# Kernel optimization log

Measured on AMD Instinct MI355X. Metric: run time of the kernel, lower is better.

Reference implementation:

```python
import jax, jax.numpy as jnp
import numpy as np

N = 1024
IN_F = 256
OUT_F = 128
H = 4
NH = OUT_F // H  # 32
NEG_SLOPE = 0.2


def setup_inputs() -> dict:
    key = jax.random.key(0)
    k1, k2, k3, k4, k5 = jax.random.split(key, 5)
    h = jax.random.normal(k1, (N, IN_F), dtype=jnp.float32)
    adj_mat = jax.random.randint(k2, (N, N, 1), 0, 2, dtype=jnp.int32)
    s_in = 1.0 / np.sqrt(IN_F)
    s_nh = 1.0 / np.sqrt(NH)
    Wl = jax.random.uniform(k3, (H * NH, IN_F), jnp.float32, -s_in, s_in)
    Wr = jax.random.uniform(k4, (H * NH, IN_F), jnp.float32, -s_in, s_in)
    attn_w = jax.random.uniform(k5, (NH,), jnp.float32, -s_nh, s_nh)
    return {"h": h, "adj_mat": adj_mat, "Wl": Wl, "Wr": Wr, "attn_w": attn_w}


def reference(h, adj_mat, Wl, Wr, attn_w):
    n = h.shape[0]
    g_l = (h @ Wl.T).reshape(n, H, NH)  # [N,H,F]
    g_r = (h @ Wr.T).reshape(n, H, NH)  # [N,H,F]
    # g_sum[i, j] = g_l[j] + g_r[i]  (repeat / repeat_interleave semantics)
    g_sum = g_l[None, :, :, :] + g_r[:, None, :, :]  # [N,N,H,F]
    act = jnp.where(g_sum >= 0, g_sum, NEG_SLOPE * g_sum)
    e = jnp.einsum('ijhf,f->ijh', act, attn_w)  # [N,N,H]
    mask = adj_mat != 0  # [N,N,1] broadcasts over heads
    e = jnp.where(mask, e, -jnp.inf)
    a = jax.nn.softmax(e, axis=1)  # softmax over source nodes j
    h_prime = jnp.einsum('ijh,jhf->ihf', a, g_r).reshape(n, H * NH)
    # is_output_layer=False -> ELU (dropout is a no-op in eval)
    return jax.nn.elu(h_prime)
```

## Files before the change

kernel.cpp:

```cpp
#include <hip/hip_runtime.h>
#include <math.h>

#define NN 1024
#define IN_F 256
#define OUT_F 128
#define NHEADS 4
#define NHF 32
#define ITILE 4
#define HPSTR 260

__global__ void __launch_bounds__(256, 4) glr_gemm(const float* __restrict__ hmat,
                                                   const float* __restrict__ Wl,
                                                   const float* __restrict__ Wr,
                                                   float* __restrict__ glh,
                                                   float* __restrict__ grh) {
    __shared__ float hp[16 * HPSTR];
    const int tid = threadIdx.x;
    const int rg = blockIdx.x & 63;
    const int cs = blockIdx.x >> 6;

    const float4* __restrict__ hsrc = (const float4*)hmat + rg * (16 * 64);
#pragma unroll
    for (int i = 0; i < 4; ++i) {
        const int v = tid + i * 256;
        const int row = v >> 6, kq = v & 63;
        *(float4*)(hp + row * HPSTR + kq * 4) = hsrc[v];
    }
    __syncthreads();

    const int lane = tid & 63;
    const int row  = lane & 15;
    const int kc   = lane >> 4;
    const int wu   = __builtin_amdgcn_readfirstlane(tid >> 6);
    const int c0   = cs * 16 + wu * 4;
    const float* __restrict__ wb = (c0 < OUT_F) ? (Wl + c0 * IN_F)
                                                : (Wr + (c0 - OUT_F) * IN_F);
    const float* __restrict__ hrow = hp + row * HPSTR + kc * 64;
    const float* __restrict__ wrow = wb + kc * 64;

    float a0 = 0.f, a1 = 0.f, a2 = 0.f, a3 = 0.f;
#pragma unroll 4
    for (int i = 0; i < 16; ++i) {
        const float4 hv = *(const float4*)(hrow + i * 4);
        const float4 w0 = *(const float4*)(wrow + 0 * IN_F + i * 4);
        const float4 w1 = *(const float4*)(wrow + 1 * IN_F + i * 4);
        const float4 w2 = *(const float4*)(wrow + 2 * IN_F + i * 4);
        const float4 w3 = *(const float4*)(wrow + 3 * IN_F + i * 4);
        a0 = fmaf(hv.x, w0.x, fmaf(hv.y, w0.y, fmaf(hv.z, w0.z, fmaf(hv.w, w0.w, a0))));
        a1 = fmaf(hv.x, w1.x, fmaf(hv.y, w1.y, fmaf(hv.z, w1.z, fmaf(hv.w, w1.w, a1))));
        a2 = fmaf(hv.x, w2.x, fmaf(hv.y, w2.y, fmaf(hv.z, w2.z, fmaf(hv.w, w2.w, a2))));
        a3 = fmaf(hv.x, w3.x, fmaf(hv.y, w3.y, fmaf(hv.z, w3.z, fmaf(hv.w, w3.w, a3))));
    }
    a0 += __shfl_xor(a0, 16); a0 += __shfl_xor(a0, 32);
    a1 += __shfl_xor(a1, 16); a1 += __shfl_xor(a1, 32);
    a2 += __shfl_xor(a2, 16); a2 += __shfl_xor(a2, 32);
    a3 += __shfl_xor(a3, 16); a3 += __shfl_xor(a3, 32);

    if (kc == 0) {
        const int cb = c0 & (OUT_F - 1);
        const int hh = cb >> 5;
        const int f  = cb & 31;
        float* __restrict__ dst = (c0 < OUT_F) ? glh : grh;
        float4 r; r.x = a0; r.y = a1; r.z = a2; r.w = a3;
        *(float4*)(dst + (hh * NN + rg * 16 + row) * NHF + f) = r;
    }
}

__global__ void __launch_bounds__(512, 8) gat_main(const float* __restrict__ glh,
                                                   const float* __restrict__ grh,
                                                   const int* __restrict__ adj,
                                                   const float* __restrict__ attn_w,
                                                   float* __restrict__ out) {
    const int hh  = blockIdx.y;
    const int i0  = blockIdx.x * ITILE;
    const int tid = threadIdx.x;

    __shared__ float p_buf[ITILE][1028];
    __shared__ float part[ITILE][16][NHF];
    __shared__ float red[ITILE][8];
    __shared__ float l_sh[ITILE];

    float lpart[ITILE];
#pragma unroll
    for (int ii = 0; ii < ITILE; ++ii) lpart[ii] = 0.f;

#pragma unroll 1
    for (int c = 0; c < 2; ++c) {
        const int j = (c << 9) + tid;
        const float* __restrict__ gp = glh + (hh * NN + j) * NHF;
        int adjv[ITILE];
#pragma unroll
        for (int ii = 0; ii < ITILE; ++ii) adjv[ii] = adj[(i0 + ii) * NN + j];

        float S[ITILE];
#pragma unroll
        for (int ii = 0; ii < ITILE; ++ii) S[ii] = 0.f;
        float alpha = 0.f;

#pragma unroll
        for (int fh = 0; fh < 2; ++fh) {
            const int fb = fh << 4;
            float g[16];
#pragma unroll
            for (int f4 = 0; f4 < 4; ++f4) {
                const float4 v = *(const float4*)(gp + fb + (f4 << 2));
                g[4 * f4 + 0] = v.x; g[4 * f4 + 1] = v.y;
                g[4 * f4 + 2] = v.z; g[4 * f4 + 3] = v.w;
            }
#pragma unroll
            for (int k = 0; k < 16; ++k) alpha = fmaf(g[k], attn_w[fb + k], alpha);
#pragma unroll
            for (int ii = 0; ii < ITILE; ++ii) {
                const float* __restrict__ grp = grh + (hh * NN + i0 + ii) * NHF + fb;
                float s = S[ii];
#pragma unroll
                for (int k = 0; k < 16; ++k)
                    s = fmaf(fabsf(g[k] + grp[k]), attn_w[fb + k], s);
                S[ii] = s;
            }
        }
#pragma unroll
        for (int ii = 0; ii < ITILE; ++ii) {
            const float e = fmaf(0.4f, S[ii], 0.6f * alpha);
            const float p = adjv[ii] ? __expf(e) : 0.f;
            p_buf[ii][j] = p;
            lpart[ii] += p;
        }
    }

    const int lane = tid & 63, wv = tid >> 6;
#pragma unroll
    for (int ii = 0; ii < ITILE; ++ii) {
        float v = lpart[ii];
#pragma unroll
        for (int d = 32; d > 0; d >>= 1) v += __shfl_xor(v, d);
        if (lane == 0) red[ii][wv] = v;
    }
    __syncthreads();
    if (tid < ITILE) {
        float l = red[tid][0];
#pragma unroll
        for (int w = 1; w < 8; ++w) l += red[tid][w];
        l_sh[tid] = l;
    }
    __syncthreads();

    const int f  = tid & 31;
    const int js = tid >> 5;
    const float* __restrict__ gp = grh + hh * NN * NHF + f;
    float o[ITILE];
#pragma unroll
    for (int ii = 0; ii < ITILE; ++ii) o[ii] = 0.f;
    const int jb = js << 6;
#pragma unroll 4
    for (int jj = 0; jj < 64; jj += 4) {
        const int j = jb + jj;
        const float g0 = gp[(j + 0) * NHF];
        const float g1 = gp[(j + 1) * NHF];
        const float g2 = gp[(j + 2) * NHF];
        const float g3 = gp[(j + 3) * NHF];
#pragma unroll
        for (int ii = 0; ii < ITILE; ++ii) {
            const float4 p4 = *(const float4*)&p_buf[ii][j];
            o[ii] = fmaf(p4.x, g0, fmaf(p4.y, g1, fmaf(p4.z, g2, fmaf(p4.w, g3, o[ii]))));
        }
    }
#pragma unroll
    for (int ii = 0; ii < ITILE; ++ii) part[ii][js][f] = o[ii];
    __syncthreads();

    if (tid < 32 * ITILE) {
        const int ii = tid >> 5, ff = tid & 31;
        float s0 = 0.f, s1 = 0.f, s2 = 0.f, s3 = 0.f;
#pragma unroll
        for (int k = 0; k < 16; k += 4) {
            s0 += part[ii][k + 0][ff];
            s1 += part[ii][k + 1][ff];
            s2 += part[ii][k + 2][ff];
            s3 += part[ii][k + 3][ff];
        }
        float s = ((s0 + s1) + (s2 + s3)) / l_sh[ii];
        const float r = (s > 0.f) ? s : (__expf(s) - 1.f);
        out[(i0 + ii) * OUT_F + hh * NHF + ff] = r;
    }
}

extern "C" void kernel_launch(void* const* d_in, const int* in_sizes, int n_in,
                              void* d_out, int out_size, void* d_ws, size_t ws_size,
                              hipStream_t stream) {
    const float* hmat = (const float*)d_in[0];
    const int*   adj  = (const int*)d_in[1];
    const float* Wl   = (const float*)d_in[2];
    const float* Wr   = (const float*)d_in[3];
    const float* aw   = (const float*)d_in[4];
    float* o          = (float*)d_out;

    float* glh = (float*)d_ws;
    float* grh = glh + NHEADS * NN * NHF;

    glr_gemm<<<dim3(1024), dim3(256), 0, stream>>>(hmat, Wl, Wr, glh, grh);
    gat_main<<<dim3(NN / ITILE, NHEADS), dim3(512), 0, stream>>>(glh, grh, adj, aw, o);
}
```

Measured before the change: 101.1 us.

## Use packed float2 FMAs across GEMM and attention kernels; halve GEMM row tile

Rewrites the inner products in both kernels with two-wide float vector types so the compiler can emit packed FP32 FMA instructions (v_pk_fma_f32), roughly halving the FMA instruction count. The projection GEMM also moves from 16 rows to 8 rows per block, which doubles the grid, splits the reduction 8 ways instead of 4, and raises the launch-bounds occupancy hint. The risks are extra register moves to pack operands and a changed floating-point summation order.

```diff
diff --git a/kernel.cpp b/kernel.cpp
--- a/kernel.cpp
+++ b/kernel.cpp
@@ -9,19 +9,21 @@
 #define ITILE 4
 #define HPSTR 260
 
-__global__ void __launch_bounds__(256, 4) glr_gemm(const float* __restrict__ hmat,
+typedef float vf2 __attribute__((ext_vector_type(2)));
+
+__global__ void __launch_bounds__(256, 8) glr_gemm(const float* __restrict__ hmat,
                                                    const float* __restrict__ Wl,
                                                    const float* __restrict__ Wr,
                                                    float* __restrict__ glh,
                                                    float* __restrict__ grh) {
-    __shared__ float hp[16 * HPSTR];
+    __shared__ float hp[8 * HPSTR];
     const int tid = threadIdx.x;
-    const int rg = blockIdx.x & 63;
-    const int cs = blockIdx.x >> 6;
-
-    const float4* __restrict__ hsrc = (const float4*)hmat + rg * (16 * 64);
-#pragma unroll
-    for (int i = 0; i < 4; ++i) {
+    const int rg = blockIdx.x & 127;
+    const int cs = blockIdx.x >> 7;
+
+    const float4* __restrict__ hsrc = (const float4*)hmat + rg * (8 * 64);
+#pragma unroll
+    for (int i = 0; i < 2; ++i) {
         const int v = tid + i * 256;
         const int row = v >> 6, kq = v & 63;
         *(float4*)(hp + row * HPSTR + kq * 4) = hsrc[v];
@@ -29,40 +31,46 @@
     __syncthreads();
 
     const int lane = tid & 63;
-    const int row  = lane & 15;
-    const int kc   = lane >> 4;
+    const int row  = lane & 7;
+    const int kc   = lane >> 3;
     const int wu   = __builtin_amdgcn_readfirstlane(tid >> 6);
     const int c0   = cs * 16 + wu * 4;
     const float* __restrict__ wb = (c0 < OUT_F) ? (Wl + c0 * IN_F)
                                                 : (Wr + (c0 - OUT_F) * IN_F);
-    const float* __restrict__ hrow = hp + row * HPSTR + kc * 64;
-    const float* __restrict__ wrow = wb + kc * 64;
-
-    float a0 = 0.f, a1 = 0.f, a2 = 0.f, a3 = 0.f;
-#pragma unroll 4
-    for (int i = 0; i < 16; ++i) {
+    const float* __restrict__ hrow = hp + row * HPSTR + kc * 32;
+    const float* __restrict__ wrow = wb + kc * 32;
+
+    vf2 a0 = {0.f, 0.f}, a1 = {0.f, 0.f}, a2 = {0.f, 0.f}, a3 = {0.f, 0.f};
+#pragma unroll 2
+    for (int i = 0; i < 8; ++i) {
         const float4 hv = *(const float4*)(hrow + i * 4);
+        const vf2 hA = {hv.x, hv.y};
+        const vf2 hB = {hv.z, hv.w};
         const float4 w0 = *(const float4*)(wrow + 0 * IN_F + i * 4);
         const float4 w1 = *(const float4*)(wrow + 1 * IN_F + i * 4);
         const float4 w2 = *(const float4*)(wrow + 2 * IN_F + i * 4);
         const float4 w3 = *(const float4*)(wrow + 3 * IN_F + i * 4);
-        a0 = fmaf(hv.x, w0.x, fmaf(hv.y, w0.y, fmaf(hv.z, w0.z, fmaf(hv.w, w0.w, a0))));
-        a1 = fmaf(hv.x, w1.x, fmaf(hv.y, w1.y, fmaf(hv.z, w1.z, fmaf(hv.w, w1.w, a1))));
-        a2 = fmaf(hv.x, w2.x, fmaf(hv.y, w2.y, fmaf(hv.z, w2.z, fmaf(hv.w, w2.w, a2))));
-        a3 = fmaf(hv.x, w3.x, fmaf(hv.y, w3.y, fmaf(hv.z, w3.z, fmaf(hv.w, w3.w, a3))));
-    }
-    a0 += __shfl_xor(a0, 16); a0 += __shfl_xor(a0, 32);
-    a1 += __shfl_xor(a1, 16); a1 += __shfl_xor(a1, 32);
-    a2 += __shfl_xor(a2, 16); a2 += __shfl_xor(a2, 32);
-    a3 += __shfl_xor(a3, 16); a3 += __shfl_xor(a3, 32);
+        a0 = hA * (vf2){w0.x, w0.y} + a0;  a0 = hB * (vf2){w0.z, w0.w} + a0;
+        a1 = hA * (vf2){w1.x, w1.y} + a1;  a1 = hB * (vf2){w1.z, w1.w} + a1;
+        a2 = hA * (vf2){w2.x, w2.y} + a2;  a2 = hB * (vf2){w2.z, w2.w} + a2;
+        a3 = hA * (vf2){w3.x, w3.y} + a3;  a3 = hB * (vf2){w3.z, w3.w} + a3;
+    }
+    float s0 = a0.x + a0.y, s1 = a1.x + a1.y, s2 = a2.x + a2.y, s3 = a3.x + a3.y;
+#pragma unroll
+    for (int d = 8; d <= 32; d <<= 1) {
+        s0 += __shfl_xor(s0, d);
+        s1 += __shfl_xor(s1, d);
+        s2 += __shfl_xor(s2, d);
+        s3 += __shfl_xor(s3, d);
+    }
 
     if (kc == 0) {
         const int cb = c0 & (OUT_F - 1);
         const int hh = cb >> 5;
         const int f  = cb & 31;
         float* __restrict__ dst = (c0 < OUT_F) ? glh : grh;
-        float4 r; r.x = a0; r.y = a1; r.z = a2; r.w = a3;
-        *(float4*)(dst + (hh * NN + rg * 16 + row) * NHF + f) = r;
+        float4 r; r.x = s0; r.y = s1; r.z = s2; r.w = s3;
+        *(float4*)(dst + (hh * NN + rg * 8 + row) * NHF + f) = r;
     }
 }
 
@@ -92,36 +100,43 @@
 #pragma unroll
         for (int ii = 0; ii < ITILE; ++ii) adjv[ii] = adj[(i0 + ii) * NN + j];
 
-        float S[ITILE];
-#pragma unroll
-        for (int ii = 0; ii < ITILE; ++ii) S[ii] = 0.f;
-        float alpha = 0.f;
+        vf2 S2[ITILE];
+#pragma unroll
+        for (int ii = 0; ii < ITILE; ++ii) S2[ii] = (vf2){0.f, 0.f};
+        vf2 alpha2 = {0.f, 0.f};
 
 #pragma unroll
         for (int fh = 0; fh < 2; ++fh) {
             const int fb = fh << 4;
-            float g[16];
-#pragma unroll
-            for (int f4 = 0; f4 < 4; ++f4) {
-                const float4 v = *(const float4*)(gp + fb + (f4 << 2));
-                g[4 * f4 + 0] = v.x; g[4 * f4 + 1] = v.y;
-                g[4 * f4 + 2] = v.z; g[4 * f4 + 3] = v.w;
+            vf2 g2[8];
+#pragma unroll
+            for (int q = 0; q < 4; ++q) {
+                const float4 v = *(const float4*)(gp + fb + (q << 2));
+                g2[2 * q + 0] = (vf2){v.x, v.y};
+                g2[2 * q + 1] = (vf2){v.z, v.w};
             }
 #pragma unroll
-            for (int k = 0; k < 16; ++k) alpha = fmaf(g[k], attn_w[fb + k], alpha);
+            for (int k2 = 0; k2 < 8; ++k2) {
+                const vf2 w2 = *(const vf2*)(attn_w + fb + 2 * k2);
+                alpha2 = g2[k2] * w2 + alpha2;
+            }
 #pragma unroll
             for (int ii = 0; ii < ITILE; ++ii) {
                 const float* __restrict__ grp = grh + (hh * NN + i0 + ii) * NHF + fb;
-                float s = S[ii];
-#pragma unroll
-                for (int k = 0; k < 16; ++k)
-                    s = fmaf(fabsf(g[k] + grp[k]), attn_w[fb + k], s);
-                S[ii] = s;
+                vf2 acc = S2[ii];
+#pragma unroll
+                for (int k2 = 0; k2 < 8; ++k2) {
+                    const vf2 s = g2[k2] + *(const vf2*)(grp + 2 * k2);
+                    vf2 a; a.x = fabsf(s.x); a.y = fabsf(s.y);
+                    acc = a * (*(const vf2*)(attn_w + fb + 2 * k2)) + acc;
+                }
+                S2[ii] = acc;
             }
         }
 #pragma unroll
         for (int ii = 0; ii < ITILE; ++ii) {
-            const float e = fmaf(0.4f, S[ii], 0.6f * alpha);
+            const float e = fmaf(0.4f, S2[ii].x + S2[ii].y,
+                                 0.6f * (alpha2.x + alpha2.y));
             const float p = adjv[ii] ? __expf(e) : 0.f;
             p_buf[ii][j] = p;
             lpart[ii] += p;
@@ -148,9 +163,9 @@
     const int f  = tid & 31;
     const int js = tid >> 5;
     const float* __restrict__ gp = grh + hh * NN * NHF + f;
-    float o[ITILE];
-#pragma unroll
-    for (int ii = 0; ii < ITILE; ++ii) o[ii] = 0.f;
+    vf2 o2[ITILE];
+#pragma unroll
+    for (int ii = 0; ii < ITILE; ++ii) o2[ii] = (vf2){0.f, 0.f};
     const int jb = js << 6;
 #pragma unroll 4
     for (int jj = 0; jj < 64; jj += 4) {
@@ -159,14 +174,17 @@
         const float g1 = gp[(j + 1) * NHF];
         const float g2 = gp[(j + 2) * NHF];
         const float g3 = gp[(j + 3) * NHF];
+        const vf2 gA = {g0, g1};
+        const vf2 gB = {g2, g3};
 #pragma unroll
         for (int ii = 0; ii < ITILE; ++ii) {
             const float4 p4 = *(const float4*)&p_buf[ii][j];
-            o[ii] = fmaf(p4.x, g0, fmaf(p4.y, g1, fmaf(p4.z, g2, fmaf(p4.w, g3, o[ii]))));
-        }
-    }
-#pragma unroll
-    for (int ii = 0; ii < ITILE; ++ii) part[ii][js][f] = o[ii];
+            o2[ii] = (vf2){p4.x, p4.y} * gA + o2[ii];
+            o2[ii] = (vf2){p4.z, p4.w} * gB + o2[ii];
+        }
+    }
+#pragma unroll
+    for (int ii = 0; ii < ITILE; ++ii) part[ii][js][f] = o2[ii].x + o2[ii].y;
     __syncthreads();
 
     if (tid < 32 * ITILE) {
@@ -198,6 +216,6 @@
     float* glh = (float*)d_ws;
     float* grh = glh + NHEADS * NN * NHF;
 
-    glr_gemm<<<dim3(1024), dim3(256), 0, stream>>>(hmat, Wl, Wr, glh, grh);
+    glr_gemm<<<dim3(2048), dim3(256), 0, stream>>>(hmat, Wl, Wr, glh, grh);
     gat_main<<<dim3(NN / ITILE, NHEADS), dim3(512), 0, stream>>>(glh, grh, adj, aw, o);
 }
```

Result: no change. 99.88 us (-1.2%).
